# Kernel optimization log

Hardware: AMD Instinct MI355X
Metric: run time of the kernel (lower is better)

Reference implementation:

```python
import jax, jax.numpy as jnp
import numpy as np

NUM_EXPERTS = 128
INPUT_DIM = 128
HIDDEN_DIM = 512
OUTPUT_DIM = 128
TOKENS_PER_EXPERT = 2048


def make_identity_experts(num_experts, input_dim, output_dim):
    # identical to the torch helper: zeros with ones on the (square) diagonal
    d = min(input_dim, output_dim)
    w = jnp.zeros((num_experts, input_dim, output_dim), dtype=jnp.float32)
    idx = jnp.arange(d)
    return w.at[:, idx, idx].set(1.0)


def setup_inputs() -> dict:
    key = jax.random.key(0)
    k_tok, = jax.random.split(key, 1)
    group_token = jax.random.normal(
        k_tok, (NUM_EXPERTS, TOKENS_PER_EXPERT, INPUT_DIM), dtype=jnp.float32)
    weights1 = make_identity_experts(NUM_EXPERTS, INPUT_DIM, HIDDEN_DIM)
    weights2 = make_identity_experts(NUM_EXPERTS, HIDDEN_DIM, OUTPUT_DIM)
    return {"group_token": group_token, "weights1": weights1, "weights2": weights2}


def reference(group_token, weights1, weights2):
    # grouped GEMM 1: per-expert [T, in] @ [in, hid]
    h = jnp.einsum('etd,edh->eth', group_token, weights1)
    # exact (erf-based) GELU, matching torch.nn.functional.gelu default
    h = jax.nn.gelu(h, approximate=False)
    # grouped GEMM 2: per-expert [T, hid] @ [hid, out]
    out = jnp.einsum('eth,eho->eto', h, weights2)
    return out
```

## Files before the change

kernel.cpp:

```cpp
#include <hip/hip_runtime.h>
#include <hip/hip_bf16.h>
#include <stdint.h>

typedef __attribute__((ext_vector_type(8))) short s8v;
typedef __attribute__((ext_vector_type(4))) short s4v;
typedef __attribute__((ext_vector_type(4))) float f4v;

#define NE   128
#define NT   2048
#define DIN  128
#define DH   512
#define DOUT 128

#define MFMA32(a,b,c) __builtin_amdgcn_mfma_f32_16x16x32_bf16(a,b,c,0,0,0)
#define MFMA16(a,b,c) __builtin_amdgcn_mfma_f32_16x16x16bf16_1k(a,b,c,0,0,0)

#define GLOAD16(g,l) __builtin_amdgcn_global_load_lds( \
    (const __attribute__((address_space(1))) void*)(g), \
    (__attribute__((address_space(3))) void*)(l), 16, 0, 0)

#define WAIT_VM(N) asm volatile("s_waitcnt vmcnt(" #N ")" ::: "memory")
#define BAR() do { asm volatile("" ::: "memory"); \
                   __builtin_amdgcn_s_barrier();  \
                   asm volatile("" ::: "memory"); } while (0)

__device__ __forceinline__ __hip_bfloat162 pk2(float a, float b) {
  float2 t; t.x = a; t.y = b;
  return __float22bfloat162_rn(t);
}

__device__ __forceinline__ s8v pack8(float4 a, float4 b) {
  union { s8v v; __hip_bfloat162 h[4]; } u;
  u.h[0] = pk2(a.x, a.y); u.h[1] = pk2(a.z, a.w);
  u.h[2] = pk2(b.x, b.y); u.h[3] = pk2(b.z, b.w);
  return u.v;
}

__device__ __forceinline__ float gelu_f(float x) {
  float x2 = x * x;
  float p  = __builtin_fmaf(x2, 0.07135481f, 1.5957691f);
  float e  = __expf(-x * p);
  return x * __builtin_amdgcn_rcpf(1.0f + e);
}

__global__ __launch_bounds__(256) void pack_w1(const float* __restrict__ W1,
                                               ushort* __restrict__ W1F) {
  const int e = blockIdx.x >> 4, t2 = blockIdx.x & 15;
  __shared__ float T[128][36];
  const int tid = threadIdx.x;
  const int d = tid >> 1, half = tid & 1;
  const float* src = W1 + (size_t)e * (DIN * DH) + (size_t)d * DH + t2 * 32 + half * 16;
  float4 v0 = *(const float4*)src;
  float4 v1 = *(const float4*)(src + 4);
  float4 v2 = *(const float4*)(src + 8);
  float4 v3 = *(const float4*)(src + 12);
  float* trow = &T[d][half * 16];
  *(float4*)(trow + 0) = v0; *(float4*)(trow + 4)  = v1;
  *(float4*)(trow + 8) = v2; *(float4*)(trow + 12) = v3;
  __syncthreads();
  const int lane = tid & 63, ks = tid >> 6;
  const int q = lane >> 4, l16 = lane & 15;
#pragma unroll
  for (int hl = 0; hl < 2; ++hl) {
    float g[8];
#pragma unroll
    for (int j = 0; j < 8; ++j) g[j] = T[ks * 32 + q * 8 + j][hl * 16 + l16];
    float4 a; a.x = g[0]; a.y = g[1]; a.z = g[2]; a.w = g[3];
    float4 b; b.x = g[4]; b.y = g[5]; b.z = g[6]; b.w = g[7];
    *(s8v*)(W1F + ((((size_t)e * 32 + t2 * 2 + hl) * 4) + ks) * 512 + lane * 8) = pack8(a, b);
  }
}

__global__ __launch_bounds__(256) void pack_w2(const float* __restrict__ W2,
                                               ushort* __restrict__ W2F) {
  const int e = blockIdx.x >> 5, ht = blockIdx.x & 31;
  __shared__ float T[16][132];
  const int tid = threadIdx.x;
  const int h = tid >> 4, c16 = tid & 15;
  const float* src = W2 + (size_t)e * (DH * DOUT) + (size_t)(ht * 16 + h) * DOUT + c16 * 8;
  float4 v0 = *(const float4*)src;
  float4 v1 = *(const float4*)(src + 4);
  float* trow = &T[h][c16 * 8];
  *(float4*)(trow + 0) = v0; *(float4*)(trow + 4) = v1;
  __syncthreads();
  const int lane = tid & 63;
  const int q = lane >> 4, l16 = lane & 15;
#pragma unroll
  for (int i = 0; i < 2; ++i) {
    int ot = (tid >> 6) + i * 4;
    float g0 = T[4 * q + 0][ot * 16 + l16];
    float g1 = T[4 * q + 1][ot * 16 + l16];
    float g2 = T[4 * q + 2][ot * 16 + l16];
    float g3 = T[4 * q + 3][ot * 16 + l16];
    union { s4v v; __hip_bfloat162 h2[2]; } u;
    u.h2[0] = pk2(g0, g1); u.h2[1] = pk2(g2, g3);
    *(s4v*)(W2F + (((size_t)e * 32 + ht) * 8 + ot) * 256 + lane * 4) = u.v;
  }
}

__global__ __launch_bounds__(256, 3) void moe_fused(
    const float* __restrict__ X, const ushort* __restrict__ W1F,
    const ushort* __restrict__ W2F, float* __restrict__ Out) {
  __shared__ __align__(16) ushort W1s[3][4096];
  __shared__ __align__(16) ushort W2s[3][4096];

  const int tid  = threadIdx.x;
  const int lane = tid & 63;
  const int wid  = tid >> 6;
  const int q    = lane >> 4;
  const int l16  = lane & 15;

  const int bid  = blockIdx.x;
  const int wk   = ((bid & 7) << 8) | (bid >> 3);
  const int e    = wk >> 4;
  const int tile = wk & 15;

  const float* Xe  = X + ((size_t)e * NT + (size_t)tile * 128) * DIN;
  const ushort* W1e = W1F + (size_t)e * 65536;
  const ushort* W2e = W2F + (size_t)e * 65536;
  float* Oe = Out + ((size_t)e * NT + (size_t)tile * 128) * DOUT;

  s8v xf[2][4];
#pragma unroll
  for (int mt = 0; mt < 2; ++mt) {
#pragma unroll
    for (int ks = 0; ks < 4; ++ks) {
      const float* p = Xe + (size_t)(wid * 32 + mt * 16 + l16) * DIN + ks * 32 + q * 8;
      float4 v0 = *(const float4*)p;
      float4 v1 = *(const float4*)(p + 4);
      xf[mt][ks] = pack8(v0, v1);
    }
  }

  const f4v zero4 = {0.0f, 0.0f, 0.0f, 0.0f};
  f4v oacc[2][8];
#pragma unroll
  for (int mt = 0; mt < 2; ++mt)
#pragma unroll
    for (int ot = 0; ot < 8; ++ot) oacc[mt][ot] = zero4;

  auto stage = [&](int chunk, int b) {
    const ushort* g1 = W1e + chunk * 4096;
    const ushort* g2 = W2e + chunk * 4096;
#pragma unroll
    for (int i = 0; i < 2; ++i) {
      int u = i * 256 + tid;
      GLOAD16(g1 + u * 8, &W1s[b][u * 8]);
      GLOAD16(g2 + u * 8, &W2s[b][u * 8]);
    }
  };

  asm volatile("" ::: "memory");

  stage(0, 0);
  stage(1, 1);

  int buf = 0;
  for (int c = 0; c < 16; ++c) {
    if (c < 14) {
      int nb = buf + 2; if (nb >= 3) nb -= 3;
      stage(c + 2, nb);
    }
    if (c < 14)       { WAIT_VM(8); }
    else if (c == 14) { WAIT_VM(4); }
    else              { WAIT_VM(0); }
    BAR();

#pragma unroll
    for (int hl = 0; hl < 2; ++hl) {
      f4v hacc[2]; hacc[0] = zero4; hacc[1] = zero4;
      s8v af[4];
#pragma unroll
      for (int ks = 0; ks < 4; ++ks)
        af[ks] = *(const s8v*)&W1s[buf][(hl * 4 + ks) * 512 + lane * 8];
      __builtin_amdgcn_s_setprio(1);
#pragma unroll
      for (int ks = 0; ks < 4; ++ks) {
        hacc[0] = MFMA32(af[ks], xf[0][ks], hacc[0]);
        hacc[1] = MFMA32(af[ks], xf[1][ks], hacc[1]);
      }
      __builtin_amdgcn_s_setprio(0);
      s4v a2[2];
#pragma unroll
      for (int mt = 0; mt < 2; ++mt) {
        union { s4v v; __hip_bfloat162 h2[2]; } u;
        u.h2[0] = pk2(gelu_f(hacc[mt][0]), gelu_f(hacc[mt][1]));
        u.h2[1] = pk2(gelu_f(hacc[mt][2]), gelu_f(hacc[mt][3]));
        a2[mt] = u.v;
      }
      s4v bfr[8];
#pragma unroll
      for (int ot = 0; ot < 8; ++ot)
        bfr[ot] = *(const s4v*)&W2s[buf][(hl * 8 + ot) * 256 + lane * 4];
      __builtin_amdgcn_s_setprio(1);
#pragma unroll
      for (int ot = 0; ot < 8; ++ot) {
        oacc[0][ot] = MFMA16(a2[0], bfr[ot], oacc[0][ot]);
        oacc[1][ot] = MFMA16(a2[1], bfr[ot], oacc[1][ot]);
      }
      __builtin_amdgcn_s_setprio(0);
    }

    BAR();
    ++buf; if (buf == 3) buf = 0;
  }

#pragma unroll
  for (int mt = 0; mt < 2; ++mt) {
    const int mb = wid * 32 + mt * 16 + 4 * q;
#pragma unroll
    for (int ot = 0; ot < 8; ++ot) {
      float* p = Oe + (size_t)mb * DOUT + ot * 16 + l16;
      p[0 * DOUT] = oacc[mt][ot][0];
      p[1 * DOUT] = oacc[mt][ot][1];
      p[2 * DOUT] = oacc[mt][ot][2];
      p[3 * DOUT] = oacc[mt][ot][3];
    }
  }
}

extern "C" void kernel_launch(void* const* d_in, const int* in_sizes, int n_in,
                              void* d_out, int out_size, void* d_ws, size_t ws_size,
                              hipStream_t stream) {
  const float* X  = (const float*)d_in[0];
  const float* W1 = (const float*)d_in[1];
  const float* W2 = (const float*)d_in[2];
  float* Out = (float*)d_out;

  ushort* W1F = (ushort*)d_ws;
  ushort* W2F = (ushort*)d_ws + (size_t)NE * 65536;

  pack_w1<<<NE * 16, 256, 0, stream>>>(W1, W1F);
  pack_w2<<<NE * 32, 256, 0, stream>>>(W2, W2F);
  moe_fused<<<NE * (NT / 128), 256, 0, stream>>>(X, W1F, W2F, Out);
}
```

Measured before the change: 347.5 us.

## Merge weight pack kernels and use double-buffered LDS for higher occupancy

Merges the two weight-packing kernels into one launch. The W1 pack now covers a full 32-row k-slice per block, looping over four column chunks. The fused MoE kernel drops from triple to double buffering of the weight chunks, which cuts LDS per block from 48KB to 32KB, and raises the launch bound to 5 waves-per-block target. This trades prefetch depth for occupancy and saves one kernel launch, at the risk of exposing more load latency per chunk and more register pressure.

```diff
diff --git a/kernel.cpp b/kernel.cpp
--- a/kernel.cpp
+++ b/kernel.cpp
@@ -43,66 +43,74 @@
   return x * __builtin_amdgcn_rcpf(1.0f + e);
 }
 
-__global__ __launch_bounds__(256) void pack_w1(const float* __restrict__ W1,
-                                               ushort* __restrict__ W1F) {
-  const int e = blockIdx.x >> 4, t2 = blockIdx.x & 15;
-  __shared__ float T[128][36];
+#define W1_BLOCKS (NE * 4)
+__global__ __launch_bounds__(256) void pack_weights(
+    const float* __restrict__ W1, const float* __restrict__ W2,
+    ushort* __restrict__ W1F, ushort* __restrict__ W2F) {
+  __shared__ __align__(16) float T[32 * 132];
   const int tid = threadIdx.x;
-  const int d = tid >> 1, half = tid & 1;
-  const float* src = W1 + (size_t)e * (DIN * DH) + (size_t)d * DH + t2 * 32 + half * 16;
-  float4 v0 = *(const float4*)src;
-  float4 v1 = *(const float4*)(src + 4);
-  float4 v2 = *(const float4*)(src + 8);
-  float4 v3 = *(const float4*)(src + 12);
-  float* trow = &T[d][half * 16];
-  *(float4*)(trow + 0) = v0; *(float4*)(trow + 4)  = v1;
-  *(float4*)(trow + 8) = v2; *(float4*)(trow + 12) = v3;
-  __syncthreads();
-  const int lane = tid & 63, ks = tid >> 6;
-  const int q = lane >> 4, l16 = lane & 15;
-#pragma unroll
-  for (int hl = 0; hl < 2; ++hl) {
-    float g[8];
-#pragma unroll
-    for (int j = 0; j < 8; ++j) g[j] = T[ks * 32 + q * 8 + j][hl * 16 + l16];
-    float4 a; a.x = g[0]; a.y = g[1]; a.z = g[2]; a.w = g[3];
-    float4 b; b.x = g[4]; b.y = g[5]; b.z = g[6]; b.w = g[7];
-    *(s8v*)(W1F + ((((size_t)e * 32 + t2 * 2 + hl) * 4) + ks) * 512 + lane * 8) = pack8(a, b);
-  }
-}
-
-__global__ __launch_bounds__(256) void pack_w2(const float* __restrict__ W2,
-                                               ushort* __restrict__ W2F) {
-  const int e = blockIdx.x >> 5, ht = blockIdx.x & 31;
-  __shared__ float T[16][132];
-  const int tid = threadIdx.x;
-  const int h = tid >> 4, c16 = tid & 15;
-  const float* src = W2 + (size_t)e * (DH * DOUT) + (size_t)(ht * 16 + h) * DOUT + c16 * 8;
-  float4 v0 = *(const float4*)src;
-  float4 v1 = *(const float4*)(src + 4);
-  float* trow = &T[h][c16 * 8];
-  *(float4*)(trow + 0) = v0; *(float4*)(trow + 4) = v1;
-  __syncthreads();
-  const int lane = tid & 63;
-  const int q = lane >> 4, l16 = lane & 15;
-#pragma unroll
-  for (int i = 0; i < 2; ++i) {
-    int ot = (tid >> 6) + i * 4;
-    float g0 = T[4 * q + 0][ot * 16 + l16];
-    float g1 = T[4 * q + 1][ot * 16 + l16];
-    float g2 = T[4 * q + 2][ot * 16 + l16];
-    float g3 = T[4 * q + 3][ot * 16 + l16];
-    union { s4v v; __hip_bfloat162 h2[2]; } u;
-    u.h2[0] = pk2(g0, g1); u.h2[1] = pk2(g2, g3);
-    *(s4v*)(W2F + (((size_t)e * 32 + ht) * 8 + ot) * 256 + lane * 4) = u.v;
-  }
-}
-
-__global__ __launch_bounds__(256, 3) void moe_fused(
+
+  if ((int)blockIdx.x < W1_BLOCKS) {
+    const int e = blockIdx.x >> 2, ks = blockIdx.x & 3;
+    const float* We = W1 + (size_t)e * (DIN * DH) + (size_t)(ks * 32) * DH;
+    const int r = tid >> 3, c0 = (tid & 7) * 16;
+    const int lane = tid & 63, wid = tid >> 6;
+    const int q = lane >> 4, l16 = lane & 15;
+    for (int hc = 0; hc < 4; ++hc) {
+      if (hc) __syncthreads();
+      const float* src = We + (size_t)r * DH + hc * 128 + c0;
+      float4 v0 = *(const float4*)(src + 0);
+      float4 v1 = *(const float4*)(src + 4);
+      float4 v2 = *(const float4*)(src + 8);
+      float4 v3 = *(const float4*)(src + 12);
+      float* t = &T[r * 132 + c0];
+      *(float4*)(t + 0) = v0; *(float4*)(t + 4)  = v1;
+      *(float4*)(t + 8) = v2; *(float4*)(t + 12) = v3;
+      __syncthreads();
+#pragma unroll
+      for (int i = 0; i < 2; ++i) {
+        const int htl = wid + 4 * i;
+        const int ht  = hc * 8 + htl;
+        float g[8];
+#pragma unroll
+        for (int j = 0; j < 8; ++j) g[j] = T[(8 * q + j) * 132 + 16 * htl + l16];
+        float4 a; a.x = g[0]; a.y = g[1]; a.z = g[2]; a.w = g[3];
+        float4 b; b.x = g[4]; b.y = g[5]; b.z = g[6]; b.w = g[7];
+        *(s8v*)(W1F + ((((size_t)e * 32 + ht) * 4) + ks) * 512 + lane * 8) = pack8(a, b);
+      }
+    }
+  } else {
+    const int bb = (int)blockIdx.x - W1_BLOCKS;
+    const int e = bb >> 5, ht = bb & 31;
+    float (*T2)[132] = (float (*)[132])T;
+    const int h = tid >> 4, c16 = tid & 15;
+    const float* src = W2 + (size_t)e * (DH * DOUT) + (size_t)(ht * 16 + h) * DOUT + c16 * 8;
+    float4 v0 = *(const float4*)src;
+    float4 v1 = *(const float4*)(src + 4);
+    float* trow = &T2[h][c16 * 8];
+    *(float4*)(trow + 0) = v0; *(float4*)(trow + 4) = v1;
+    __syncthreads();
+    const int lane = tid & 63;
+    const int q = lane >> 4, l16 = lane & 15;
+#pragma unroll
+    for (int i = 0; i < 2; ++i) {
+      int ot = (tid >> 6) + i * 4;
+      float g0 = T2[4 * q + 0][ot * 16 + l16];
+      float g1 = T2[4 * q + 1][ot * 16 + l16];
+      float g2 = T2[4 * q + 2][ot * 16 + l16];
+      float g3 = T2[4 * q + 3][ot * 16 + l16];
+      union { s4v v; __hip_bfloat162 h2[2]; } u;
+      u.h2[0] = pk2(g0, g1); u.h2[1] = pk2(g2, g3);
+      *(s4v*)(W2F + (((size_t)e * 32 + ht) * 8 + ot) * 256 + lane * 4) = u.v;
+    }
+  }
+}
+
+__global__ __launch_bounds__(256, 5) void moe_fused(
     const float* __restrict__ X, const ushort* __restrict__ W1F,
     const ushort* __restrict__ W2F, float* __restrict__ Out) {
-  __shared__ __align__(16) ushort W1s[3][4096];
-  __shared__ __align__(16) ushort W2s[3][4096];
+  __shared__ __align__(16) ushort W1s[2][4096];
+  __shared__ __align__(16) ushort W2s[2][4096];
 
   const int tid  = threadIdx.x;
   const int lane = tid & 63;
@@ -153,17 +161,11 @@
   asm volatile("" ::: "memory");
 
   stage(0, 0);
-  stage(1, 1);
-
-  int buf = 0;
+
   for (int c = 0; c < 16; ++c) {
-    if (c < 14) {
-      int nb = buf + 2; if (nb >= 3) nb -= 3;
-      stage(c + 2, nb);
-    }
-    if (c < 14)       { WAIT_VM(8); }
-    else if (c == 14) { WAIT_VM(4); }
-    else              { WAIT_VM(0); }
+    const int buf = c & 1;
+    if (c < 15) stage(c + 1, buf ^ 1);
+    if (c < 15) { WAIT_VM(4); } else { WAIT_VM(0); }
     BAR();
 
 #pragma unroll
@@ -202,7 +204,6 @@
     }
 
     BAR();
-    ++buf; if (buf == 3) buf = 0;
   }
 
 #pragma unroll
@@ -230,7 +231,6 @@
   ushort* W1F = (ushort*)d_ws;
   ushort* W2F = (ushort*)d_ws + (size_t)NE * 65536;
 
-  pack_w1<<<NE * 16, 256, 0, stream>>>(W1, W1F);
-  pack_w2<<<NE * 32, 256, 0, stream>>>(W2, W2F);
+  pack_weights<<<NE * 4 + NE * 32, 256, 0, stream>>>(W1, W2, W1F, W2F);
   moe_fused<<<NE * (NT / 128), 256, 0, stream>>>(X, W1F, W2F, Out);
 }
```

Result: slower. 1.080 ms (+210.9%).
